# Performance work log

Measured on AMD Instinct MI355X. Metric: run time of the kernel, lower is better.

## Reference

```python
import jax, jax.numpy as jnp
import numpy as np

B, T, C = 2, 2048, 2048
N_HEAD = 16
HEAD_DIM = C // N_HEAD


def setup_inputs() -> dict:
    key = jax.random.key(0)
    ks = jax.random.split(key, 5)
    s = 1.0 / np.sqrt(C)
    return {
        "x": jax.random.normal(ks[0], (B, T, C), dtype=jnp.float32),
        "Wq": jax.random.normal(ks[1], (C, C), dtype=jnp.float32) * s,
        "bq": jnp.zeros((C,), dtype=jnp.float32),
        "Wk": jax.random.normal(ks[2], (C, C), dtype=jnp.float32) * s,
        "bk": jnp.zeros((C,), dtype=jnp.float32),
        "Wv": jax.random.normal(ks[3], (C, C), dtype=jnp.float32) * s,
        "bv": jnp.zeros((C,), dtype=jnp.float32),
        "Wp": jax.random.normal(ks[4], (C, C), dtype=jnp.float32) * s,
        "bp": jnp.zeros((C,), dtype=jnp.float32),
    }


def reference(x, Wq, bq, Wk, bk, Wv, bv, Wp, bp):
    Bx, Tx, Cx = x.shape
    # torch nn.Linear: y = x @ W.T + b
    def lin(x, W, b):
        return jnp.einsum("btc,dc->btd", x, W) + b

    def split_heads(y):  # (B,T,C) -> (B,H,T,hd)
        return y.reshape(Bx, Tx, N_HEAD, HEAD_DIM).transpose(0, 2, 1, 3)

    q = split_heads(lin(x, Wq, bq))
    k = split_heads(lin(x, Wk, bk))
    v = split_heads(lin(x, Wv, bv))

    scale = 1.0 / np.sqrt(HEAD_DIM).astype(np.float32)
    attn = jnp.einsum("bhqd,bhkd->bhqk", q, k) * scale  # (B,H,T,T)
    causal = jnp.tril(jnp.ones((Tx, Tx), dtype=bool))
    attn = jnp.where(causal[None, None], attn, -jnp.inf)
    attn = jax.nn.softmax(attn, axis=-1)
    out = jnp.einsum("bhqk,bhkd->bhqd", attn, v)  # (B,H,T,hd)
    # Faithful to original: transpose(-2,-1) swaps T and head_dim, then
    # a contiguous view reinterprets memory as (B,T,C).
    out = out.transpose(0, 1, 3, 2).reshape(Bx, Tx, Cx)
    return lin(out, Wp, bp)
```

## Files before the change

### kernel.cpp

```cpp
#include <hip/hip_runtime.h>
#include <stdint.h>

#define DEVI __device__ __forceinline__

typedef __attribute__((ext_vector_type(8))) short short8;
typedef __attribute__((ext_vector_type(4))) float f32x4;
typedef __attribute__((ext_vector_type(4))) unsigned int u32x4;

static constexpr int Bn = 2;
static constexpr int Tn = 2048;
static constexpr int Cn = 2048;
static constexpr int NH = 16;
static constexpr int HD = 128;
static constexpr int Kdim = 2048;

DEVI unsigned short f2bf(float f) {
  union { float f; unsigned u; } v; v.f = f;
  return (unsigned short)((v.u + 0x7FFFu + ((v.u >> 16) & 1u)) >> 16);
}

DEVI void gload_lds16(const void* g, void* l) {
  __builtin_amdgcn_global_load_lds(
      (const __attribute__((address_space(1))) void*)g,
      (__attribute__((address_space(3))) void*)l, 16, 0, 0);
}

__global__ __launch_bounds__(256) void cast_bf16_kernel(
    const float* __restrict__ src, unsigned short* __restrict__ dst, int n) {
  int idx = (blockIdx.x * blockDim.x + threadIdx.x) * 4;
  const int stride = gridDim.x * blockDim.x * 4;
  for (; idx < n; idx += stride) {
    f32x4 f = *(const f32x4*)(src + idx);
    unsigned short o[4];
    o[0] = f2bf(f[0]); o[1] = f2bf(f[1]); o[2] = f2bf(f[2]); o[3] = f2bf(f[3]);
    *(unsigned long long*)(dst + idx) = *(const unsigned long long*)o;
  }
}

__global__ __launch_bounds__(256) void cast4_kernel(
    const float* __restrict__ s0, const float* __restrict__ s1,
    const float* __restrict__ s2, const float* __restrict__ s3,
    unsigned short* __restrict__ d0, unsigned short* __restrict__ d1,
    unsigned short* __restrict__ d2, unsigned short* __restrict__ d3, int n) {
  const int w = blockIdx.y;
  const float* src = (w == 0) ? s0 : (w == 1) ? s1 : (w == 2) ? s2 : s3;
  unsigned short* dst = (w == 0) ? d0 : (w == 1) ? d1 : (w == 2) ? d2 : d3;
  int idx = (blockIdx.x * blockDim.x + threadIdx.x) * 4;
  const int stride = gridDim.x * blockDim.x * 4;
  for (; idx < n; idx += stride) {
    f32x4 f = *(const f32x4*)(src + idx);
    unsigned short o[4];
    o[0] = f2bf(f[0]); o[1] = f2bf(f[1]); o[2] = f2bf(f[2]); o[3] = f2bf(f[3]);
    *(unsigned long long*)(dst + idx) = *(const unsigned long long*)o;
  }
}

#define G_BAR() __builtin_amdgcn_s_barrier()
#define G_MFMA(d, a, b) d = __builtin_amdgcn_mfma_f32_16x16x32_bf16(a, b, d, 0, 0, 0)

__global__ __launch_bounds__(512, 2) void gemm_qkv_256x192_kernel(
    const unsigned short* __restrict__ X,
    const unsigned short* __restrict__ W3,
    const float* __restrict__ bq_, const float* __restrict__ bk_, const float* __restrict__ bv_,
    unsigned short* __restrict__ Qo, unsigned short* __restrict__ Ko,
    unsigned short* __restrict__ Vo) {
  constexpr int NT = Kdim / 64;
  __shared__ unsigned short L[2][28672];

  const int tid = threadIdx.x;
  const int wave = tid >> 6, lane = tid & 63;
  const int wm = wave >> 2, wn = wave & 3;
  const int quad = lane >> 4, lr = lane & 15;

  const int flat = (int)blockIdx.x + 32 * (int)blockIdx.y;
  const int swz = (flat & 7) * 64 + (flat >> 3);
  const int bx = swz & 31, by = swz >> 5;
  const int n0 = bx * 192;
  const int m0 = by * 256;

  f32x4 acc[8][3];
  const f32x4 zero4 = {0.f, 0.f, 0.f, 0.f};
#pragma unroll
  for (int i = 0; i < 8; ++i)
#pragma unroll
    for (int j = 0; j < 3; ++j) acc[i][j] = zero4;

  const int srow = tid >> 3;
  const int schunk = (tid & 7) ^ (srow & 7);
  const unsigned short* Asrc = X + (size_t)(m0 + srow) * Kdim + schunk * 8;
  const unsigned short* Bsrc = W3 + (size_t)(n0 + srow) * Kdim + schunk * 8;

  auto STAGE_A = [&](int buf, int t) {
    unsigned short* d = &L[buf][tid * 8];
    const unsigned short* s = Asrc + t * 64;
#pragma unroll
    for (int h = 0; h < 4; ++h)
      gload_lds16(s + (size_t)(h * 64) * Kdim, d + h * 4096);
  };
  auto STAGE_B = [&](int buf, int t) {
    unsigned short* d = &L[buf][16384 + tid * 8];
    const unsigned short* s = Bsrc + t * 64;
#pragma unroll
    for (int h = 0; h < 3; ++h)
      gload_lds16(s + (size_t)(h * 64) * Kdim, d + h * 4096);
  };

  const int pc0 = quad ^ (lr & 7);
  const int pc1 = (4 + quad) ^ (lr & 7);
  const int aoff = (wm * 128 + lr) * 64;
  const int boff = 16384 + (wn * 48 + lr) * 64;

  STAGE_A(0, 0);
  STAGE_B(0, 0);
  STAGE_B(1, 1);
  asm volatile("s_waitcnt vmcnt(3)" ::: "memory");
  G_BAR();

  short8 Af[4][2], Bf[3][2];

  for (int t = 0; t < NT; ++t) {
    const int cur = t & 1, nxt = cur ^ 1;
#pragma unroll
    for (int m = 0; m < 4; ++m) {
      Af[m][0] = *(const short8*)&L[cur][aoff + m * 1024 + pc0 * 8];
      Af[m][1] = *(const short8*)&L[cur][aoff + m * 1024 + pc1 * 8];
    }
#pragma unroll
    for (int n = 0; n < 3; ++n) {
      Bf[n][0] = *(const short8*)&L[cur][boff + n * 1024 + pc0 * 8];
      Bf[n][1] = *(const short8*)&L[cur][boff + n * 1024 + pc1 * 8];
    }
    if (t + 1 < NT) STAGE_A(nxt, t + 1);
    G_BAR();
    __builtin_amdgcn_s_setprio(1);
#pragma unroll
    for (int m = 0; m < 4; ++m)
#pragma unroll
      for (int n = 0; n < 3; ++n) {
        G_MFMA(acc[m][n], Af[m][0], Bf[n][0]);
        G_MFMA(acc[m][n], Af[m][1], Bf[n][1]);
      }
    __builtin_amdgcn_s_setprio(0);
    G_BAR();
#pragma unroll
    for (int m = 0; m < 4; ++m) {
      Af[m][0] = *(const short8*)&L[cur][aoff + (m + 4) * 1024 + pc0 * 8];
      Af[m][1] = *(const short8*)&L[cur][aoff + (m + 4) * 1024 + pc1 * 8];
    }
    if (t + 2 < NT) STAGE_B(cur, t + 2);
    G_BAR();
    __builtin_amdgcn_s_setprio(1);
#pragma unroll
    for (int m = 0; m < 4; ++m)
#pragma unroll
      for (int n = 0; n < 3; ++n) {
        G_MFMA(acc[m + 4][n], Af[m][0], Bf[n][0]);
        G_MFMA(acc[m + 4][n], Af[m][1], Bf[n][1]);
      }
    __builtin_amdgcn_s_setprio(0);
    if (t < NT - 2) { asm volatile("s_waitcnt vmcnt(3)" ::: "memory"); }
    else            { asm volatile("s_waitcnt vmcnt(0)" ::: "memory"); }
    G_BAR();
  }

#pragma unroll
  for (int ni = 0; ni < 3; ++ni) {
    const int n = n0 + wn * 48 + ni * 16 + lr;
    const int mat = n >> 11;
    const int nl = n & 2047;
    const int h = nl >> 7, d = nl & 127;
    const float bv = (mat == 0 ? bq_ : mat == 1 ? bk_ : bv_)[nl];
    if (mat == 2) {
#pragma unroll
      for (int mi = 0; mi < 8; ++mi) {
        const int m = m0 + wm * 128 + mi * 16 + quad * 4;
        const int b = m >> 11, tt = m & 2047;
        unsigned short o4[4];
#pragma unroll
        for (int r = 0; r < 4; ++r) o4[r] = f2bf(acc[mi][ni][r] + bv);
        *(unsigned long long*)&Vo[(((size_t)(b * NH + h)) * HD + d) * Tn + tt] =
            *(const unsigned long long*)o4;
      }
    } else {
      unsigned short* Out = (mat == 0) ? Qo : Ko;
#pragma unroll
      for (int mi = 0; mi < 8; ++mi) {
#pragma unroll
        for (int r = 0; r < 4; ++r) {
          const int m = m0 + wm * 128 + mi * 16 + quad * 4 + r;
          const int b = m >> 11, tt = m & 2047;
          Out[(((size_t)(b * NH + h)) * Tn + tt) * HD + d] = f2bf(acc[mi][ni][r] + bv);
        }
      }
    }
  }
}

__global__ __launch_bounds__(512, 2) void gemm_proj_256x128_kernel(
    const unsigned short* __restrict__ Aall,
    const unsigned short* __restrict__ Wp_,
    const float* __restrict__ bias,
    float* __restrict__ Y) {
  constexpr int NT = Kdim / 64;
  __shared__ unsigned short L[2][24576];

  const int tid = threadIdx.x;
  const int wave = tid >> 6, lane = tid & 63;
  const int wm = wave >> 2, wn = wave & 3;
  const int quad = lane >> 4, lr = lane & 15;

  const int flat = (int)blockIdx.x + 16 * (int)blockIdx.y;
  const int swz = (flat & 7) * 16 + (flat >> 3);
  const int bx = swz % 16, by = swz / 16;
  const int m0 = by * 256, n0 = bx * 128;
  const int bz = blockIdx.z;
  const unsigned short* A = Aall + (size_t)bz * Cn * Tn;

  f32x4 acc[8][2];
  const f32x4 zero4 = {0.f, 0.f, 0.f, 0.f};
#pragma unroll
  for (int i = 0; i < 8; ++i)
#pragma unroll
    for (int j = 0; j < 2; ++j) acc[i][j] = zero4;

  const int srow = tid >> 3;
  const int schunk = (tid & 7) ^ (srow & 7);
  const unsigned short* Asrc = A + (size_t)(m0 + srow) * Kdim + schunk * 8;
  const unsigned short* Bsrc = Wp_ + (size_t)(n0 + srow) * Kdim + schunk * 8;

  auto STAGE_A = [&](int buf, int h, int t) {
    unsigned short* d = &L[buf][h * 8192 + tid * 8];
    const unsigned short* s = Asrc + (size_t)(h * 128) * Kdim + t * 64;
    gload_lds16(s, d);
    gload_lds16(s + (size_t)64 * Kdim, d + 4096);
  };
  auto STAGE_B = [&](int buf, int t) {
    unsigned short* d = &L[buf][16384 + tid * 8];
    const unsigned short* s = Bsrc + t * 64;
    gload_lds16(s, d);
    gload_lds16(s + (size_t)64 * Kdim, d + 4096);
  };

  const int pc0 = quad ^ (lr & 7);
  const int pc1 = (4 + quad) ^ (lr & 7);
  const int aoff = (wm * 128 + lr) * 64;
  const int boff = 16384 + (wn * 32 + lr) * 64;

  STAGE_A(0, 0, 0); STAGE_A(0, 1, 0);
  STAGE_B(0, 0);
  STAGE_B(1, 1);
  asm volatile("s_waitcnt vmcnt(2)" ::: "memory");
  G_BAR();

  short8 Af[4][2], Bf[2][2];

  for (int t = 0; t < NT; ++t) {
    const int cur = t & 1, nxt = cur ^ 1;
#pragma unroll
    for (int m = 0; m < 4; ++m) {
      Af[m][0] = *(const short8*)&L[cur][aoff + m * 1024 + pc0 * 8];
      Af[m][1] = *(const short8*)&L[cur][aoff + m * 1024 + pc1 * 8];
    }
#pragma unroll
    for (int n = 0; n < 2; ++n) {
      Bf[n][0] = *(const short8*)&L[cur][boff + n * 1024 + pc0 * 8];
      Bf[n][1] = *(const short8*)&L[cur][boff + n * 1024 + pc1 * 8];
    }
    if (t + 1 < NT) STAGE_A(nxt, 0, t + 1);
    G_BAR();
    __builtin_amdgcn_s_setprio(1);
#pragma unroll
    for (int m = 0; m < 4; ++m)
#pragma unroll
      for (int n = 0; n < 2; ++n) {
        G_MFMA(acc[m][n], Af[m][0], Bf[n][0]);
        G_MFMA(acc[m][n], Af[m][1], Bf[n][1]);
      }
    __builtin_amdgcn_s_setprio(0);
    G_BAR();
#pragma unroll
    for (int m = 0; m < 4; ++m) {
      Af[m][0] = *(const short8*)&L[cur][aoff + (m + 4) * 1024 + pc0 * 8];
      Af[m][1] = *(const short8*)&L[cur][aoff + (m + 4) * 1024 + pc1 * 8];
    }
    if (t + 1 < NT) STAGE_A(nxt, 1, t + 1);
    if (t + 2 < NT) STAGE_B(cur, t + 2);
    G_BAR();
    __builtin_amdgcn_s_setprio(1);
#pragma unroll
    for (int m = 0; m < 4; ++m)
#pragma unroll
      for (int n = 0; n < 2; ++n) {
        G_MFMA(acc[m + 4][n], Af[m][0], Bf[n][0]);
        G_MFMA(acc[m + 4][n], Af[m][1], Bf[n][1]);
      }
    __builtin_amdgcn_s_setprio(0);
    if (t < NT - 2) { asm volatile("s_waitcnt vmcnt(2)" ::: "memory"); }
    else            { asm volatile("s_waitcnt vmcnt(0)" ::: "memory"); }
    G_BAR();
  }

#pragma unroll
  for (int ni = 0; ni < 2; ++ni) {
    const int n = n0 + wn * 32 + ni * 16 + lr;
    const float bv = bias[n];
#pragma unroll
    for (int mi = 0; mi < 8; ++mi) {
#pragma unroll
      for (int r = 0; r < 4; ++r) {
        const int m = m0 + wm * 128 + mi * 16 + quad * 4 + r;
        Y[((size_t)bz * Tn + m) * Cn + n] = acc[mi][ni][r] + bv;
      }
    }
  }
}

__global__ __launch_bounds__(256, 1) void attn_kernel(
    const unsigned short* __restrict__ Q,
    const unsigned short* __restrict__ K,
    const unsigned short* __restrict__ V,
    unsigned short* __restrict__ Ot) {
  constexpr int KST = 136;
  constexpr int VST = 136;
  constexpr int PST = 136;
  __shared__ unsigned short Ks[128 * KST];
  __shared__ unsigned short Vs[144 * VST];
  __shared__ unsigned short Ps[128 * PST];

  const int tid = threadIdx.x;
  const int wave = tid >> 6, lane = tid & 63;
  const int quad = lane >> 4, lr = lane & 15;
  const int bh = blockIdx.y;
  const float SL = 0.08838834764831845f * 1.4426950408889634f;

  const unsigned short* Kp = K + (size_t)bh * Tn * HD;
  const unsigned short* Vp = V + (size_t)bh * HD * Tn;
  unsigned short* Pw = &Ps[wave * 32 * PST];

  for (int i = tid; i < 16 * VST; i += 256) Vs[128 * VST + i] = 0x3F80;

  const int r = tid >> 1;
  const int cc = (tid & 1) * 64;
  unsigned short* kl = &Ks[r * KST + cc];
  unsigned short* vl = &Vs[r * VST + cc];
  u32x4 kreg[8], vreg[8];

  const f32x4 zero4 = {0.f, 0.f, 0.f, 0.f};
#pragma unroll 1
  for (int half = 0; half < 2; ++half) {
    const int jt = half ? (15 - (int)blockIdx.x) : (int)blockIdx.x;
    const int q0 = jt * 128;

    const unsigned short* Qp = Q + ((size_t)bh * Tn + q0 + wave * 32) * HD;
    short8 qf[2][4];
#pragma unroll
    for (int mi = 0; mi < 2; ++mi)
#pragma unroll
      for (int ks = 0; ks < 4; ++ks)
        qf[mi][ks] = *(const short8*)&Qp[(mi * 16 + lr) * HD + ks * 32 + quad * 8];

    f32x4 oacc[2][9];
#pragma unroll
    for (int mi = 0; mi < 2; ++mi)
#pragma unroll
      for (int nd = 0; nd < 9; ++nd) oacc[mi][nd] = zero4;

    const int nch = q0 / 128 + 1;

    {
      const unsigned short* kg = &Kp[(size_t)r * HD + cc];
      const unsigned short* vg = &Vp[(size_t)r * Tn + cc];
#pragma unroll
      for (int p = 0; p < 8; ++p) {
        kreg[p] = *(const u32x4*)(kg + p * 8);
        vreg[p] = *(const u32x4*)(vg + p * 8);
      }
    }

    for (int c = 0; c < nch; ++c) {
      const int k0 = c * 128;
#pragma unroll
      for (int p = 0; p < 8; ++p) {
        *(u32x4*)(kl + p * 8) = kreg[p];
        *(u32x4*)(vl + p * 8) = vreg[p];
      }
      __syncthreads();
      if (c + 1 < nch) {
        const int k1 = k0 + 128;
        const unsigned short* kg = &Kp[(size_t)(k1 + r) * HD + cc];
        const unsigned short* vg = &Vp[(size_t)r * Tn + k1 + cc];
#pragma unroll
        for (int p = 0; p < 8; ++p) {
          kreg[p] = *(const u32x4*)(kg + p * 8);
          vreg[p] = *(const u32x4*)(vg + p * 8);
        }
      }

      f32x4 sa[2][8];
#pragma unroll
      for (int mi = 0; mi < 2; ++mi)
#pragma unroll
        for (int nt = 0; nt < 8; ++nt) sa[mi][nt] = zero4;
#pragma unroll
      for (int nt = 0; nt < 8; ++nt) {
        short8 kf[4];
#pragma unroll
        for (int ks = 0; ks < 4; ++ks)
          kf[ks] = *(const short8*)&Ks[(nt * 16 + lr) * KST + ks * 32 + quad * 8];
#pragma unroll
        for (int mi = 0; mi < 2; ++mi)
#pragma unroll
          for (int ks = 0; ks < 4; ++ks)
            sa[mi][nt] = __builtin_amdgcn_mfma_f32_16x16x32_bf16(qf[mi][ks], kf[ks], sa[mi][nt], 0, 0, 0);
      }

      if (k0 == q0) {
#pragma unroll
        for (int mi = 0; mi < 2; ++mi)
#pragma unroll
          for (int nt = 0; nt < 8; ++nt)
#pragma unroll
            for (int r2 = 0; r2 < 4; ++r2) {
              const int qg = q0 + wave * 32 + mi * 16 + quad * 4 + r2;
              const int kg = k0 + nt * 16 + lr;
              if (kg > qg) sa[mi][nt][r2] = -3.0e38f;
            }
      }

#pragma unroll
      for (int mi = 0; mi < 2; ++mi)
#pragma unroll
        for (int nt = 0; nt < 8; ++nt)
#pragma unroll
          for (int r2 = 0; r2 < 4; ++r2) {
            const float p = __builtin_amdgcn_exp2f(sa[mi][nt][r2] * SL);
            Pw[(mi * 16 + quad * 4 + r2) * PST + nt * 16 + lr] = f2bf(p);
          }

#pragma unroll
      for (int kt = 0; kt < 4; ++kt) {
        short8 pf[2];
#pragma unroll
        for (int mi = 0; mi < 2; ++mi)
          pf[mi] = *(const short8*)&Pw[(mi * 16 + lr) * PST + kt * 32 + quad * 8];
#pragma unroll
        for (int nd = 0; nd < 9; ++nd) {
          short8 vf = *(const short8*)&Vs[(nd * 16 + lr) * VST + kt * 32 + quad * 8];
#pragma unroll
          for (int mi = 0; mi < 2; ++mi)
            oacc[mi][nd] = __builtin_amdgcn_mfma_f32_16x16x32_bf16(pf[mi], vf, oacc[mi][nd], 0, 0, 0);
        }
      }
      __syncthreads();
    }

#pragma unroll
    for (int mi = 0; mi < 2; ++mi)
#pragma unroll
      for (int r2 = 0; r2 < 4; ++r2) {
        const float rl = 1.0f / oacc[mi][8][r2];
        const int tl = wave * 32 + mi * 16 + quad * 4 + r2;
#pragma unroll
        for (int nd = 0; nd < 8; ++nd)
          Ps[tl * PST + nd * 16 + lr] = f2bf(oacc[mi][nd][r2] * rl);
      }
    __syncthreads();
    {
      unsigned short* Od = Ot + (size_t)bh * HD * Tn + q0;
#pragma unroll
      for (int p = 0; p < 8; ++p) {
        const int d = p * 16 + (tid >> 4);
        const int t8 = (tid & 15) * 8;
        alignas(16) unsigned short v[8];
#pragma unroll
        for (int j = 0; j < 8; ++j) v[j] = Ps[(t8 + j) * PST + d];
        *(u32x4*)&Od[(size_t)d * Tn + t8] = *(const u32x4*)v;
      }
    }
    __syncthreads();
  }
}

extern "C" void kernel_launch(void* const* d_in, const int* in_sizes, int n_in,
                              void* d_out, int out_size, void* d_ws, size_t ws_size,
                              hipStream_t stream) {
  const float* x  = (const float*)d_in[0];
  const float* Wq = (const float*)d_in[1];
  const float* bq = (const float*)d_in[2];
  const float* Wk = (const float*)d_in[3];
  const float* bk = (const float*)d_in[4];
  const float* Wv = (const float*)d_in[5];
  const float* bv = (const float*)d_in[6];
  const float* Wp = (const float*)d_in[7];
  const float* bp = (const float*)d_in[8];
  float* out = (float*)d_out;

  char* ws = (char*)d_ws;
  const size_t MB = 1ull << 20;
  unsigned short* Xbf = (unsigned short*)(ws);
  unsigned short* Wqb = (unsigned short*)(ws + 16 * MB);
  unsigned short* Wkb = (unsigned short*)(ws + 24 * MB);
  unsigned short* Wvb = (unsigned short*)(ws + 32 * MB);
  unsigned short* Wpb = (unsigned short*)(ws + 40 * MB);
  unsigned short* Qb  = (unsigned short*)(ws + 48 * MB);
  unsigned short* Kb  = (unsigned short*)(ws + 64 * MB);
  unsigned short* Vtb = (unsigned short*)(ws + 80 * MB);
  unsigned short* Otb = (unsigned short*)(ws + 96 * MB);

  cast_bf16_kernel<<<dim3(1024), dim3(256), 0, stream>>>(x, Xbf, Bn * Tn * Cn);
  cast4_kernel<<<dim3(512, 4), dim3(256), 0, stream>>>(
      Wq, Wk, Wv, Wp, Wqb, Wkb, Wvb, Wpb, Cn * Cn);

  gemm_qkv_256x192_kernel<<<dim3(32, 16), dim3(512), 0, stream>>>(
      Xbf, Wqb , bq, bk, bv, Qb, Kb, Vtb);

  attn_kernel<<<dim3(8, Bn * NH), dim3(256), 0, stream>>>(Qb, Kb, Vtb, Otb);

  gemm_proj_256x128_kernel<<<dim3(16, 8, 2), dim3(512), 0, stream>>>(
      Otb, Wpb, bp, out);
}
```

Before: 395.9 us.

## Split attention key chunks across two wave groups with LDS reduction

Doubles the attention block to 512 threads. Each group of four waves computes half of every 128-key chunk's scores and P·V products, and the two groups' partial output accumulators are summed through shared memory at the end of each query tile. The aim is more waves per CU to hide MFMA and memory latency on a grid of only 256 blocks. In exchange it adds a cross-wave reduction through LDS, re-zero-fills the ones-row in V for each half, and halves the per-thread load work.

```diff
diff --git a/kernel.cpp b/kernel.cpp
--- a/kernel.cpp
+++ b/kernel.cpp
@@ -315,7 +315,7 @@
   }
 }
 
-__global__ __launch_bounds__(256, 1) void attn_kernel(
+__global__ __launch_bounds__(512, 2) void attn_kernel(
     const unsigned short* __restrict__ Q,
     const unsigned short* __restrict__ K,
     const unsigned short* __restrict__ V,
@@ -323,27 +323,28 @@
   constexpr int KST = 136;
   constexpr int VST = 136;
   constexpr int PST = 136;
-  __shared__ unsigned short Ks[128 * KST];
-  __shared__ unsigned short Vs[144 * VST];
-  __shared__ unsigned short Ps[128 * PST];
+  __shared__ unsigned short SMEM[54400];
+  unsigned short* Ks = SMEM;
+  unsigned short* Vs = SMEM + 17408;
+  unsigned short* Ps = SMEM + 36992;
 
   const int tid = threadIdx.x;
   const int wave = tid >> 6, lane = tid & 63;
+  const int wb = wave & 3;
+  const int wh = wave >> 2;
   const int quad = lane >> 4, lr = lane & 15;
   const int bh = blockIdx.y;
   const float SL = 0.08838834764831845f * 1.4426950408889634f;
 
   const unsigned short* Kp = K + (size_t)bh * Tn * HD;
   const unsigned short* Vp = V + (size_t)bh * HD * Tn;
-  unsigned short* Pw = &Ps[wave * 32 * PST];
-
-  for (int i = tid; i < 16 * VST; i += 256) Vs[128 * VST + i] = 0x3F80;
-
-  const int r = tid >> 1;
-  const int cc = (tid & 1) * 64;
+  unsigned short* Pw = &Ps[wb * 32 * PST];
+
+  const int r = tid >> 2;
+  const int cc = (tid & 3) * 32;
   unsigned short* kl = &Ks[r * KST + cc];
   unsigned short* vl = &Vs[r * VST + cc];
-  u32x4 kreg[8], vreg[8];
+  u32x4 kreg[4], vreg[4];
 
   const f32x4 zero4 = {0.f, 0.f, 0.f, 0.f};
 #pragma unroll 1
@@ -351,7 +352,9 @@
     const int jt = half ? (15 - (int)blockIdx.x) : (int)blockIdx.x;
     const int q0 = jt * 128;
 
-    const unsigned short* Qp = Q + ((size_t)bh * Tn + q0 + wave * 32) * HD;
+    for (int i = tid; i < 16 * VST; i += 512) Vs[128 * VST + i] = 0x3F80;
+
+    const unsigned short* Qp = Q + ((size_t)bh * Tn + q0 + wb * 32) * HD;
     short8 qf[2][4];
 #pragma unroll
     for (int mi = 0; mi < 2; ++mi)
@@ -371,7 +374,7 @@
       const unsigned short* kg = &Kp[(size_t)r * HD + cc];
       const unsigned short* vg = &Vp[(size_t)r * Tn + cc];
 #pragma unroll
-      for (int p = 0; p < 8; ++p) {
+      for (int p = 0; p < 4; ++p) {
         kreg[p] = *(const u32x4*)(kg + p * 8);
         vreg[p] = *(const u32x4*)(vg + p * 8);
       }
@@ -380,7 +383,7 @@
     for (int c = 0; c < nch; ++c) {
       const int k0 = c * 128;
 #pragma unroll
-      for (int p = 0; p < 8; ++p) {
+      for (int p = 0; p < 4; ++p) {
         *(u32x4*)(kl + p * 8) = kreg[p];
         *(u32x4*)(vl + p * 8) = vreg[p];
       }
@@ -390,19 +393,20 @@
         const unsigned short* kg = &Kp[(size_t)(k1 + r) * HD + cc];
         const unsigned short* vg = &Vp[(size_t)r * Tn + k1 + cc];
 #pragma unroll
-        for (int p = 0; p < 8; ++p) {
+        for (int p = 0; p < 4; ++p) {
           kreg[p] = *(const u32x4*)(kg + p * 8);
           vreg[p] = *(const u32x4*)(vg + p * 8);
         }
       }
 
-      f32x4 sa[2][8];
+      f32x4 sa[2][4];
 #pragma unroll
       for (int mi = 0; mi < 2; ++mi)
 #pragma unroll
-        for (int nt = 0; nt < 8; ++nt) sa[mi][nt] = zero4;
-#pragma unroll
-      for (int nt = 0; nt < 8; ++nt) {
+        for (int n4 = 0; n4 < 4; ++n4) sa[mi][n4] = zero4;
+#pragma unroll
+      for (int n4 = 0; n4 < 4; ++n4) {
+        const int nt = wh * 4 + n4;
         short8 kf[4];
 #pragma unroll
         for (int ks = 0; ks < 4; ++ks)
@@ -411,34 +415,35 @@
         for (int mi = 0; mi < 2; ++mi)
 #pragma unroll
           for (int ks = 0; ks < 4; ++ks)
-            sa[mi][nt] = __builtin_amdgcn_mfma_f32_16x16x32_bf16(qf[mi][ks], kf[ks], sa[mi][nt], 0, 0, 0);
+            sa[mi][n4] = __builtin_amdgcn_mfma_f32_16x16x32_bf16(qf[mi][ks], kf[ks], sa[mi][n4], 0, 0, 0);
       }
 
       if (k0 == q0) {
 #pragma unroll
         for (int mi = 0; mi < 2; ++mi)
 #pragma unroll
-          for (int nt = 0; nt < 8; ++nt)
+          for (int n4 = 0; n4 < 4; ++n4)
 #pragma unroll
             for (int r2 = 0; r2 < 4; ++r2) {
-              const int qg = q0 + wave * 32 + mi * 16 + quad * 4 + r2;
-              const int kg = k0 + nt * 16 + lr;
-              if (kg > qg) sa[mi][nt][r2] = -3.0e38f;
+              const int qg = q0 + wb * 32 + mi * 16 + quad * 4 + r2;
+              const int kg = k0 + (wh * 4 + n4) * 16 + lr;
+              if (kg > qg) sa[mi][n4][r2] = -3.0e38f;
             }
       }
 
 #pragma unroll
       for (int mi = 0; mi < 2; ++mi)
 #pragma unroll
-        for (int nt = 0; nt < 8; ++nt)
+        for (int n4 = 0; n4 < 4; ++n4)
 #pragma unroll
           for (int r2 = 0; r2 < 4; ++r2) {
-            const float p = __builtin_amdgcn_exp2f(sa[mi][nt][r2] * SL);
-            Pw[(mi * 16 + quad * 4 + r2) * PST + nt * 16 + lr] = f2bf(p);
+            const float p = __builtin_amdgcn_exp2f(sa[mi][n4][r2] * SL);
+            Pw[(mi * 16 + quad * 4 + r2) * PST + (wh * 4 + n4) * 16 + lr] = f2bf(p);
           }
 
 #pragma unroll
-      for (int kt = 0; kt < 4; ++kt) {
+      for (int k2 = 0; k2 < 2; ++k2) {
+        const int kt = wh * 2 + k2;
         short8 pf[2];
 #pragma unroll
         for (int mi = 0; mi < 2; ++mi)
@@ -454,18 +459,34 @@
       __syncthreads();
     }
 
-#pragma unroll
-    for (int mi = 0; mi < 2; ++mi)
-#pragma unroll
-      for (int r2 = 0; r2 < 4; ++r2) {
-        const float rl = 1.0f / oacc[mi][8][r2];
-        const int tl = wave * 32 + mi * 16 + quad * 4 + r2;
-#pragma unroll
-        for (int nd = 0; nd < 8; ++nd)
-          Ps[tl * PST + nd * 16 + lr] = f2bf(oacc[mi][nd][r2] * rl);
-      }
+    f32x4* cbuf = (f32x4*)SMEM;
+    if (wh == 1) {
+#pragma unroll
+      for (int mi = 0; mi < 2; ++mi)
+#pragma unroll
+        for (int nd = 0; nd < 9; ++nd)
+          cbuf[(wb * 64 + lane) * 18 + mi * 9 + nd] = oacc[mi][nd];
+    }
     __syncthreads();
-    {
+    if (wh == 0) {
+#pragma unroll
+      for (int mi = 0; mi < 2; ++mi)
+#pragma unroll
+        for (int nd = 0; nd < 9; ++nd)
+          oacc[mi][nd] += cbuf[(wb * 64 + lane) * 18 + mi * 9 + nd];
+#pragma unroll
+      for (int mi = 0; mi < 2; ++mi)
+#pragma unroll
+        for (int r2 = 0; r2 < 4; ++r2) {
+          const float rl = 1.0f / oacc[mi][8][r2];
+          const int tl = wb * 32 + mi * 16 + quad * 4 + r2;
+#pragma unroll
+          for (int nd = 0; nd < 8; ++nd)
+            Ps[tl * PST + nd * 16 + lr] = f2bf(oacc[mi][nd][r2] * rl);
+        }
+    }
+    __syncthreads();
+    if (tid < 256) {
       unsigned short* Od = Ot + (size_t)bh * HD * Tn + q0;
 #pragma unroll
       for (int p = 0; p < 8; ++p) {
@@ -514,7 +535,7 @@
   gemm_qkv_256x192_kernel<<<dim3(32, 16), dim3(512), 0, stream>>>(
       Xbf, Wqb , bq, bk, bv, Qb, Kb, Vtb);
 
-  attn_kernel<<<dim3(8, Bn * NH), dim3(256), 0, stream>>>(Qb, Kb, Vtb, Otb);
+  attn_kernel<<<dim3(8, Bn * NH), dim3(512), 0, stream>>>(Qb, Kb, Vtb, Otb);
 
   gemm_proj_256x128_kernel<<<dim3(16, 8, 2), dim3(512), 0, stream>>>(
       Otb, Wpb, bp, out);
```

Measured after the change: 373.2 us. 1.06x faster.
